# Performance work log

Hardware: AMD Instinct MI355X
Metric: run time of the kernel (lower is better)

## Reference

```python
import jax, jax.numpy as jnp
import numpy as np

N, K, D, L = 4096, 64, 1024, 16384  # tokens, top-k, d_in, num_latents


def setup_inputs() -> dict:
    key = jax.random.key(0)
    ks = jax.random.split(key, 9)
    x = jax.random.normal(ks[0], (N, D), jnp.float32)
    y = jax.random.normal(ks[1], (N, D), jnp.float32)
    latent_acts = jax.random.uniform(ks[2], (N, K), jnp.float32)  # post-topk acts (nonneg)
    latent_indices = jax.random.randint(ks[3], (N, K), 0, L)
    W_dec = jax.random.normal(ks[4], (L, D), jnp.float32) / np.sqrt(D).astype(np.float32)
    b_dec = jax.random.normal(ks[5], (D,), jnp.float32) * 0.01
    post_enc = jax.random.normal(ks[6], (L,), jnp.float32) * 0.01
    post_enc_scale = 1.0 + 0.1 * jax.random.normal(ks[7], (L,), jnp.float32)
    W_skip = jax.random.normal(ks[8], (D, D), jnp.float32) / np.sqrt(D).astype(np.float32)
    return {
        "x": x, "y": y,
        "latent_acts": latent_acts, "latent_indices": latent_indices,
        "W_dec": W_dec, "b_dec": b_dec,
        "post_enc": post_enc, "post_enc_scale": post_enc_scale,
        "W_skip": W_skip,
    }


def reference(x, y, latent_acts, latent_indices, W_dec, b_dec, post_enc, post_enc_scale, W_skip):
    # current_latent_acts: per-index bias gather + indexed scaling
    acts = (latent_acts + post_enc[latent_indices]) * post_enc_scale[latent_indices]  # [N,K]
    # decode: gather W_dec rows by top-k indices, weighted combine, add decoder bias
    sae_out = jnp.einsum('nk,nkd->nd', acts, W_dec[latent_indices]) + b_dec  # [N,D]
    # skip connection: x @ W_skip.mT
    sae_out = sae_out + x @ W_skip.T
    # FVU loss
    e = y - sae_out
    total_variance = jnp.sum((y - jnp.mean(y, axis=0)) ** 2)
    fvu = jnp.sum(e ** 2) / total_variance
    return sae_out, fvu
```

## Files before the change

kernel.cpp:

```cpp
#include <hip/hip_runtime.h>
#include <hip/hip_bf16.h>
#include <cstdint>

#define N_TOK 4096
#define KTOP  64
#define DIM   1024
#define NLAT  16384
#define NCHUNK 8

typedef __bf16 bf16x8 __attribute__((ext_vector_type(8)));
typedef float  floatx4 __attribute__((ext_vector_type(4)));
typedef float  f32x4   __attribute__((ext_vector_type(4)));
typedef unsigned int   u32x2   __attribute__((ext_vector_type(2)));

#define GLOBAL_AS(p) ((const __attribute__((address_space(1))) void*)(p))
#define LDS_AS(p)    ((__attribute__((address_space(3))) void*)(p))

__device__ inline unsigned short f2bf(float f){
  unsigned int u = __float_as_uint(f);
  unsigned int r = (u + 0x7fffu + ((u >> 16) & 1u)) >> 16;
  return (unsigned short)r;
}
__device__ inline float bflo(unsigned int u){ return __uint_as_float(u << 16); }
__device__ inline float bfhi(unsigned int u){ return __uint_as_float(u & 0xffff0000u); }

__device__ inline ushort4 cvt4(float4 v){
  ushort4 o; o.x = f2bf(v.x); o.y = f2bf(v.y); o.z = f2bf(v.z); o.w = f2bf(v.w);
  return o;
}

__global__ __launch_bounds__(256) void prep(
    const float* __restrict__ x, const float* __restrict__ Wsk,
    const float* __restrict__ Wd, const float* __restrict__ y,
    const float* __restrict__ la, const int* __restrict__ li,
    const float* __restrict__ pe, const float* __restrict__ pes,
    unsigned short* __restrict__ xb, unsigned short* __restrict__ wb,
    unsigned short* __restrict__ wdc,
    uint2* __restrict__ actbuf, float* __restrict__ accs){
  const int b = blockIdx.x;
  const int t = threadIdx.x;
  __shared__ float s_red[4];
  if (b < 128){
    const int r0 = b * 32;
    const float4* y4 = (const float4*)y;
    float4 cs = {0.f, 0.f, 0.f, 0.f};
    float sq = 0.f;
    #pragma unroll
    for (int g = 0; g < 8; g++){
      float4 v0 = y4[(size_t)(r0 + g*4 + 0) * 256 + t];
      float4 v1 = y4[(size_t)(r0 + g*4 + 1) * 256 + t];
      float4 v2 = y4[(size_t)(r0 + g*4 + 2) * 256 + t];
      float4 v3 = y4[(size_t)(r0 + g*4 + 3) * 256 + t];
      cs.x += v0.x + v1.x + v2.x + v3.x;
      cs.y += v0.y + v1.y + v2.y + v3.y;
      cs.z += v0.z + v1.z + v2.z + v3.z;
      cs.w += v0.w + v1.w + v2.w + v3.w;
      sq += v0.x*v0.x + v0.y*v0.y + v0.z*v0.z + v0.w*v0.w;
      sq += v1.x*v1.x + v1.y*v1.y + v1.z*v1.z + v1.w*v1.w;
      sq += v2.x*v2.x + v2.y*v2.y + v2.z*v2.z + v2.w*v2.w;
      sq += v3.x*v3.x + v3.y*v3.y + v3.z*v3.z + v3.w*v3.w;
    }
    atomicAdd(&accs[4 + t*4 + 0], cs.x);
    atomicAdd(&accs[4 + t*4 + 1], cs.y);
    atomicAdd(&accs[4 + t*4 + 2], cs.z);
    atomicAdd(&accs[4 + t*4 + 3], cs.w);
    #pragma unroll
    for (int off = 32; off > 0; off >>= 1) sq += __shfl_down(sq, off, 64);
    if ((t & 63) == 0) s_red[t >> 6] = sq;
    __syncthreads();
    if (t == 0) atomicAdd(&accs[1], s_red[0] + s_red[1] + s_red[2] + s_red[3]);
  } else if (b < 640){
    const float4* xs = (const float4*)x;
    ushort4* xd = (ushort4*)xb;
    const int i0 = (b - 128) * 2048 + t;
    float4 v[8];
    #pragma unroll
    for (int i = 0; i < 8; i++) v[i] = xs[i0 + i * 256];
    #pragma unroll
    for (int i = 0; i < 8; i++) xd[i0 + i * 256] = cvt4(v[i]);
  } else if (b < 768){
    const float4* ws = (const float4*)Wsk;
    ushort4* wd2 = (ushort4*)wb;
    const int i0 = (b - 640) * 2048 + t;
    float4 v[8];
    #pragma unroll
    for (int i = 0; i < 8; i++) v[i] = ws[i0 + i * 256];
    #pragma unroll
    for (int i = 0; i < 8; i++) wd2[i0 + i * 256] = cvt4(v[i]);
  } else if (b < 2816){
    const int r0 = (b - 768) * 8;
    const float4* ws = (const float4*)Wd;
    float4 v[8];
    #pragma unroll
    for (int r = 0; r < 8; r++) v[r] = ws[(size_t)(r0 + r) * 256 + t];
    const int chunk = t >> 5;
    const int off   = (t & 31) * 4;
    #pragma unroll
    for (int r = 0; r < 8; r++)
      *(ushort4*)(wdc + ((size_t)chunk * NLAT + r0 + r) * 128 + off) = cvt4(v[r]);
  } else {
    int e0 = (b - 2816) * 4096 + t;
    #pragma unroll
    for (int i = 0; i < 16; i++){
      int e = e0 + i * 256;
      int id = li[e];
      float a = (la[e] + pe[id]) * pes[id];
      actbuf[e] = make_uint2(__float_as_uint(a), (unsigned)id * 256u);
    }
  }
}

__global__ __launch_bounds__(256) void skip_gemm(
    const unsigned short* __restrict__ xb,
    const unsigned short* __restrict__ wb,
    const float* __restrict__ b_dec,
    float* __restrict__ out){
  __shared__ unsigned short As[128][32];
  __shared__ unsigned short Bs[64][32];
  const int row0 = blockIdx.x * 128;
  const int col0 = blockIdx.y * 64;
  const int t    = threadIdx.x;
  const int lane = t & 63;
  const int w    = t >> 6;
  const int wr   = w * 32;
  const int lm   = lane & 15;
  const int kq   = lane >> 4;
  const int sr   = t >> 2;
  const int sc   = (t & 3) * 8;

  floatx4 acc[2][4] = {};

  for (int k0 = 0; k0 < DIM; k0 += 32){
    __builtin_amdgcn_global_load_lds(GLOBAL_AS(xb + (size_t)(row0 + sr) * DIM + k0 + sc),
                                     LDS_AS(&As[sr][sc]), 16, 0, 0);
    __builtin_amdgcn_global_load_lds(GLOBAL_AS(xb + (size_t)(row0 + 64 + sr) * DIM + k0 + sc),
                                     LDS_AS(&As[64 + sr][sc]), 16, 0, 0);
    __builtin_amdgcn_global_load_lds(GLOBAL_AS(wb + (size_t)(col0 + sr) * DIM + k0 + sc),
                                     LDS_AS(&Bs[sr][sc]), 16, 0, 0);
    __syncthreads();
    bf16x8 af[2], bfr[4];
    #pragma unroll
    for (int mi = 0; mi < 2; mi++) af[mi] = *(const bf16x8*)(&As[wr + mi * 16 + lm][kq * 8]);
    #pragma unroll
    for (int ni = 0; ni < 4; ni++) bfr[ni] = *(const bf16x8*)(&Bs[ni * 16 + lm][kq * 8]);
    #pragma unroll
    for (int mi = 0; mi < 2; mi++)
      #pragma unroll
      for (int ni = 0; ni < 4; ni++)
        acc[mi][ni] = __builtin_amdgcn_mfma_f32_16x16x32_bf16(af[mi], bfr[ni], acc[mi][ni], 0, 0, 0);
    __syncthreads();
  }

  const int rq = (lane >> 4) * 4;
  #pragma unroll
  for (int mi = 0; mi < 2; mi++){
    #pragma unroll
    for (int ni = 0; ni < 4; ni++){
      int col = col0 + ni * 16 + lm;
      float bd = b_dec[col];
      #pragma unroll
      for (int r = 0; r < 4; r++){
        int row = row0 + wr + mi * 16 + rq + r;
        out[(size_t)row * DIM + col] = acc[mi][ni][r] + bd;
      }
    }
  }
}

__global__ __launch_bounds__(256) void decode_residual(
    const float* __restrict__ y,
    const uint2* __restrict__ actbuf,
    const unsigned short* __restrict__ Wdc,
    float* __restrict__ out,
    float* __restrict__ sse){
  const int chunk = blockIdx.x & 7;
  const int tok0  = (blockIdx.x >> 3) * 16;
  const int t  = threadIdx.x;
  const int tl = t >> 4;
  const int cl = t & 15;
  __shared__ uint2 s_ai[16][66];
  __shared__ float s_red[4];

  #pragma unroll
  for (int i = 0; i < 4; i++){
    int e = t + i * 256;
    u32x2 v = __builtin_nontemporal_load((const u32x2*)&actbuf[tok0 * KTOP + e]);
    s_ai[e >> 6][e & 63] = make_uint2(v[0], v[1]);
  }
  __syncthreads();
  const int n = tok0 + tl;
  const char* Wbase = (const char*)Wdc + (size_t)chunk * NLAT * 256 + cl * 16;
  float* op = out + (size_t)n * DIM + chunk * 128 + cl * 8;
  const float* yp = y + (size_t)n * DIM + chunk * 128 + cl * 8;
  f32x4 o0 = __builtin_nontemporal_load((const f32x4*)op);
  f32x4 o1 = __builtin_nontemporal_load((const f32x4*)op + 1);
  f32x4 y0 = __builtin_nontemporal_load((const f32x4*)yp);
  f32x4 y1 = __builtin_nontemporal_load((const f32x4*)yp + 1);

  float acc[8] = {};
  #pragma unroll 16
  for (int k = 0; k < KTOP; k++){
    uint2 p = s_ai[tl][k];
    const float a = __uint_as_float(p.x);
    const uint4 wv = *(const uint4*)(Wbase + p.y);
    acc[0] += a * bflo(wv.x); acc[1] += a * bfhi(wv.x);
    acc[2] += a * bflo(wv.y); acc[3] += a * bfhi(wv.y);
    acc[4] += a * bflo(wv.z); acc[5] += a * bfhi(wv.z);
    acc[6] += a * bflo(wv.w); acc[7] += a * bfhi(wv.w);
  }
  acc[0] += o0[0]; acc[1] += o0[1]; acc[2] += o0[2]; acc[3] += o0[3];
  acc[4] += o1[0]; acc[5] += o1[1]; acc[6] += o1[2]; acc[7] += o1[3];
  f32x4 r0 = {acc[0], acc[1], acc[2], acc[3]};
  f32x4 r1 = {acc[4], acc[5], acc[6], acc[7]};
  __builtin_nontemporal_store(r0, (f32x4*)op);
  __builtin_nontemporal_store(r1, (f32x4*)op + 1);

  float e0 = y0[0]-acc[0], e1 = y0[1]-acc[1], e2 = y0[2]-acc[2], e3 = y0[3]-acc[3];
  float e4 = y1[0]-acc[4], e5 = y1[1]-acc[5], e6 = y1[2]-acc[6], e7 = y1[3]-acc[7];
  float s = e0*e0 + e1*e1 + e2*e2 + e3*e3 + e4*e4 + e5*e5 + e6*e6 + e7*e7;
  #pragma unroll
  for (int off = 32; off > 0; off >>= 1) s += __shfl_down(s, off, 64);
  if ((t & 63) == 0) s_red[t >> 6] = s;
  __syncthreads();
  if (t == 0) atomicAdd(sse, s_red[0] + s_red[1] + s_red[2] + s_red[3]);
}

__global__ __launch_bounds__(256) void fvu_kernel(
    const float* __restrict__ ws, float* __restrict__ fvu_out){
  const int t = threadIdx.x;
  float4 c = ((const float4*)(ws + 4))[t];
  float s = c.x*c.x + c.y*c.y + c.z*c.z + c.w*c.w;
  #pragma unroll
  for (int off = 32; off > 0; off >>= 1) s += __shfl_down(s, off, 64);
  __shared__ float s_red[4];
  if ((t & 63) == 0) s_red[t >> 6] = s;
  __syncthreads();
  if (t == 0){
    float ss = s_red[0] + s_red[1] + s_red[2] + s_red[3];
    float tv = ws[1] - ss / (float)N_TOK;
    fvu_out[0] = ws[0] / tv;
  }
}

extern "C" void kernel_launch(void* const* d_in, const int* in_sizes, int n_in,
                              void* d_out, int out_size, void* d_ws, size_t ws_size,
                              hipStream_t stream){
  const float* x   = (const float*)d_in[0];
  const float* y   = (const float*)d_in[1];
  const float* la  = (const float*)d_in[2];
  const int*   li  = (const int*)d_in[3];
  const float* Wd  = (const float*)d_in[4];
  const float* bd  = (const float*)d_in[5];
  const float* pe  = (const float*)d_in[6];
  const float* pes = (const float*)d_in[7];
  const float* Wsk = (const float*)d_in[8];
  float* out = (float*)d_out;

  float* accs = (float*)d_ws;
  unsigned short* xb  = (unsigned short*)((char*)d_ws + 8192);
  unsigned short* wb  = xb + (size_t)N_TOK * DIM;
  unsigned short* wdc = wb + (size_t)DIM * DIM;
  uint2* actbuf = (uint2*)(wdc + (size_t)NCHUNK * NLAT * 128);

  hipMemsetAsync(d_ws, 0, 8192, stream);
  prep<<<2880, 256, 0, stream>>>(x, Wsk, Wd, y, la, li, pe, pes, xb, wb, wdc, actbuf, accs);
  skip_gemm<<<dim3(N_TOK / 128, DIM / 64), 256, 0, stream>>>(xb, wb, bd, out);
  decode_residual<<<(N_TOK / 16) * NCHUNK, 256, 0, stream>>>(y, actbuf, wdc, out, accs);
  fvu_kernel<<<1, 256, 0, stream>>>(accs, out + (size_t)N_TOK * DIM);
}
```

Measured before the change: 242.1 us.

## Restructure prep: row-major W_dec copy, move y stats into skip GEMM, drop memset

The conversion blocks now use a shared routine with 8-element bf16 stores and non-temporal loads. W_dec is kept row-major in bf16 instead of chunk-major, so the decode gather reads a row offset (id*2048) plus a chunk offset. The y column-sum and sum-of-squares pass moves from prep into extra blocks of the skip GEMM launch so it runs alongside the GEMM. The workspace memset is replaced by a zeroing block in prep. The aim is to cut launch count and make the prep kernel a lighter pure-conversion pass. In exchange, the decode gather now touches rows with a 2 KB stride, which may change cache behaviour.

```diff
diff --git a/kernel.cpp b/kernel.cpp
--- a/kernel.cpp
+++ b/kernel.cpp
@@ -12,6 +12,7 @@
 typedef float  floatx4 __attribute__((ext_vector_type(4)));
 typedef float  f32x4   __attribute__((ext_vector_type(4)));
 typedef unsigned int   u32x2   __attribute__((ext_vector_type(2)));
+typedef unsigned short ushortx8 __attribute__((ext_vector_type(8)));
 
 #define GLOBAL_AS(p) ((const __attribute__((address_space(1))) void*)(p))
 #define LDS_AS(p)    ((__attribute__((address_space(3))) void*)(p))
@@ -24,24 +25,74 @@
 __device__ inline float bflo(unsigned int u){ return __uint_as_float(u << 16); }
 __device__ inline float bfhi(unsigned int u){ return __uint_as_float(u & 0xffff0000u); }
 
-__device__ inline ushort4 cvt4(float4 v){
-  ushort4 o; o.x = f2bf(v.x); o.y = f2bf(v.y); o.z = f2bf(v.z); o.w = f2bf(v.w);
+__device__ inline ushortx8 cvt8p(f32x4 a, f32x4 b){
+  ushortx8 o;
+  o[0] = f2bf(a[0]); o[1] = f2bf(a[1]); o[2] = f2bf(a[2]); o[3] = f2bf(a[3]);
+  o[4] = f2bf(b[0]); o[5] = f2bf(b[1]); o[6] = f2bf(b[2]); o[7] = f2bf(b[3]);
   return o;
+}
+
+__device__ inline void cvt_rows8(const f32x4* __restrict__ src, ushortx8* __restrict__ dst,
+                                 int r0, int t){
+  const int co = t & 127;
+  const int lr = t >> 7;
+  f32x4 va[4], vb[4];
+  #pragma unroll
+  for (int s = 0; s < 4; s++){
+    const size_t row = r0 + s*2 + lr;
+    va[s] = __builtin_nontemporal_load(src + row*256 + 2*co);
+    vb[s] = __builtin_nontemporal_load(src + row*256 + 2*co + 1);
+  }
+  __builtin_amdgcn_sched_barrier(0);
+  #pragma unroll
+  for (int s = 0; s < 4; s++){
+    const size_t row = r0 + s*2 + lr;
+    dst[row*128 + co] = cvt8p(va[s], vb[s]);
+  }
 }
 
 __global__ __launch_bounds__(256) void prep(
     const float* __restrict__ x, const float* __restrict__ Wsk,
-    const float* __restrict__ Wd, const float* __restrict__ y,
+    const float* __restrict__ Wd,
     const float* __restrict__ la, const int* __restrict__ li,
     const float* __restrict__ pe, const float* __restrict__ pes,
     unsigned short* __restrict__ xb, unsigned short* __restrict__ wb,
-    unsigned short* __restrict__ wdc,
+    unsigned short* __restrict__ wdb,
     uint2* __restrict__ actbuf, float* __restrict__ accs){
   const int b = blockIdx.x;
   const int t = threadIdx.x;
-  __shared__ float s_red[4];
-  if (b < 128){
-    const int r0 = b * 32;
+  if (b < 512){
+    cvt_rows8((const f32x4*)x, (ushortx8*)xb, b * 8, t);
+  } else if (b < 640){
+    cvt_rows8((const f32x4*)Wsk, (ushortx8*)wb, (b - 512) * 8, t);
+  } else if (b < 2688){
+    cvt_rows8((const f32x4*)Wd, (ushortx8*)wdb, (b - 640) * 8, t);
+  } else if (b < 2752){
+    int e0 = (b - 2688) * 4096 + t;
+    #pragma unroll
+    for (int i = 0; i < 16; i++){
+      int e = e0 + i * 256;
+      int id = li[e];
+      float a = (la[e] + pe[id]) * pes[id];
+      actbuf[e] = make_uint2(__float_as_uint(a), (unsigned)id * 2048u);
+    }
+  } else {
+    for (int i = t; i < 1056; i += 256) accs[i] = 0.f;
+  }
+}
+
+__global__ __launch_bounds__(256) void skip_gemm(
+    const unsigned short* __restrict__ xb,
+    const unsigned short* __restrict__ wb,
+    const float* __restrict__ b_dec,
+    const float* __restrict__ y,
+    float* __restrict__ out,
+    float* __restrict__ accs){
+  const int t = threadIdx.x;
+  if (blockIdx.x >= 32){
+    __shared__ float s_red[4];
+    const int yb = (blockIdx.x - 32) * 16 + blockIdx.y;
+    const int r0 = yb * 32;
     const float4* y4 = (const float4*)y;
     float4 cs = {0.f, 0.f, 0.f, 0.f};
     float sq = 0.f;
@@ -69,57 +120,12 @@
     if ((t & 63) == 0) s_red[t >> 6] = sq;
     __syncthreads();
     if (t == 0) atomicAdd(&accs[1], s_red[0] + s_red[1] + s_red[2] + s_red[3]);
-  } else if (b < 640){
-    const float4* xs = (const float4*)x;
-    ushort4* xd = (ushort4*)xb;
-    const int i0 = (b - 128) * 2048 + t;
-    float4 v[8];
-    #pragma unroll
-    for (int i = 0; i < 8; i++) v[i] = xs[i0 + i * 256];
-    #pragma unroll
-    for (int i = 0; i < 8; i++) xd[i0 + i * 256] = cvt4(v[i]);
-  } else if (b < 768){
-    const float4* ws = (const float4*)Wsk;
-    ushort4* wd2 = (ushort4*)wb;
-    const int i0 = (b - 640) * 2048 + t;
-    float4 v[8];
-    #pragma unroll
-    for (int i = 0; i < 8; i++) v[i] = ws[i0 + i * 256];
-    #pragma unroll
-    for (int i = 0; i < 8; i++) wd2[i0 + i * 256] = cvt4(v[i]);
-  } else if (b < 2816){
-    const int r0 = (b - 768) * 8;
-    const float4* ws = (const float4*)Wd;
-    float4 v[8];
-    #pragma unroll
-    for (int r = 0; r < 8; r++) v[r] = ws[(size_t)(r0 + r) * 256 + t];
-    const int chunk = t >> 5;
-    const int off   = (t & 31) * 4;
-    #pragma unroll
-    for (int r = 0; r < 8; r++)
-      *(ushort4*)(wdc + ((size_t)chunk * NLAT + r0 + r) * 128 + off) = cvt4(v[r]);
-  } else {
-    int e0 = (b - 2816) * 4096 + t;
-    #pragma unroll
-    for (int i = 0; i < 16; i++){
-      int e = e0 + i * 256;
-      int id = li[e];
-      float a = (la[e] + pe[id]) * pes[id];
-      actbuf[e] = make_uint2(__float_as_uint(a), (unsigned)id * 256u);
-    }
-  }
-}
-
-__global__ __launch_bounds__(256) void skip_gemm(
-    const unsigned short* __restrict__ xb,
-    const unsigned short* __restrict__ wb,
-    const float* __restrict__ b_dec,
-    float* __restrict__ out){
+    return;
+  }
   __shared__ unsigned short As[128][32];
   __shared__ unsigned short Bs[64][32];
   const int row0 = blockIdx.x * 128;
   const int col0 = blockIdx.y * 64;
-  const int t    = threadIdx.x;
   const int lane = t & 63;
   const int w    = t >> 6;
   const int wr   = w * 32;
@@ -170,7 +176,7 @@
 __global__ __launch_bounds__(256) void decode_residual(
     const float* __restrict__ y,
     const uint2* __restrict__ actbuf,
-    const unsigned short* __restrict__ Wdc,
+    const unsigned short* __restrict__ Wdb,
     float* __restrict__ out,
     float* __restrict__ sse){
   const int chunk = blockIdx.x & 7;
@@ -189,7 +195,7 @@
   }
   __syncthreads();
   const int n = tok0 + tl;
-  const char* Wbase = (const char*)Wdc + (size_t)chunk * NLAT * 256 + cl * 16;
+  const char* Wbase = (const char*)Wdb + chunk * 256 + cl * 16;
   float* op = out + (size_t)n * DIM + chunk * 128 + cl * 8;
   const float* yp = y + (size_t)n * DIM + chunk * 128 + cl * 8;
   f32x4 o0 = __builtin_nontemporal_load((const f32x4*)op);
@@ -259,12 +265,11 @@
   float* accs = (float*)d_ws;
   unsigned short* xb  = (unsigned short*)((char*)d_ws + 8192);
   unsigned short* wb  = xb + (size_t)N_TOK * DIM;
-  unsigned short* wdc = wb + (size_t)DIM * DIM;
-  uint2* actbuf = (uint2*)(wdc + (size_t)NCHUNK * NLAT * 128);
-
-  hipMemsetAsync(d_ws, 0, 8192, stream);
-  prep<<<2880, 256, 0, stream>>>(x, Wsk, Wd, y, la, li, pe, pes, xb, wb, wdc, actbuf, accs);
-  skip_gemm<<<dim3(N_TOK / 128, DIM / 64), 256, 0, stream>>>(xb, wb, bd, out);
-  decode_residual<<<(N_TOK / 16) * NCHUNK, 256, 0, stream>>>(y, actbuf, wdc, out, accs);
+  unsigned short* wdb = wb + (size_t)DIM * DIM;
+  uint2* actbuf = (uint2*)(wdb + (size_t)NLAT * DIM);
+
+  prep<<<2753, 256, 0, stream>>>(x, Wsk, Wd, la, li, pe, pes, xb, wb, wdb, actbuf, accs);
+  skip_gemm<<<dim3(40, 16), 256, 0, stream>>>(xb, wb, bd, y, out, accs);
+  decode_residual<<<(N_TOK / 16) * NCHUNK, 256, 0, stream>>>(y, actbuf, wdb, out, accs);
   fvu_kernel<<<1, 256, 0, stream>>>(accs, out + (size_t)N_TOK * DIM);
 }
```

After: 242.2 us. About the same (+0.1%).
